# Kernel tuning notes

Measured on AMD Instinct MI355X. Metric: run time of the kernel, lower is better.

The kernel has to match this reference:

```python
import jax, jax.numpy as jnp
import numpy as np

N = 50000
E = 1600000
D_CONTENT, D_STYLE, D_CAT = 768, 128, 32  # concat feature = 2*D_CAT = 64
H1, H2, NCLS = 64, 64, 2


def _lin_params(key, din, dout, bias=True):
    k1, k2 = jax.random.split(key)
    s = 1.0 / np.sqrt(din)
    W = jax.random.uniform(k1, (din, dout), jnp.float32, -s, s)
    b = jax.random.uniform(k2, (dout,), jnp.float32, -s, s) if bias else None
    return W, b


def setup_inputs() -> dict:
    key = jax.random.key(0)
    ks = jax.random.split(key, 16)
    x_content = jax.random.normal(ks[0], (N, D_CONTENT), jnp.float32)
    x_style = jax.random.normal(ks[1], (N, D_STYLE), jnp.float32)
    edge_index = jax.random.randint(ks[2], (2, E), 0, N, jnp.int64)
    edge_type = jax.random.randint(ks[3], (E,), 0, 4, jnp.int64)
    Wp, bp = _lin_params(ks[4], D_CONTENT, D_CAT)
    Ws, bs = _lin_params(ks[5], D_STYLE, D_CAT)
    # SAGEConv: lin_l (aggregated neighbors, has bias), lin_r (root, no bias)
    Wl1, bl1 = _lin_params(ks[6], 2 * D_CAT, H1)
    Wr1, _ = _lin_params(ks[7], 2 * D_CAT, H1, bias=False)
    Wl2, bl2 = _lin_params(ks[8], H1, H2)
    Wr2, _ = _lin_params(ks[9], H1, H2, bias=False)
    Wl3, bl3 = _lin_params(ks[10], H2, H2)
    Wr3, _ = _lin_params(ks[11], H2, H2, bias=False)
    Wo, bo = _lin_params(ks[12], H2, NCLS)
    return dict(x_content=x_content, x_style=x_style, edge_index=edge_index,
                edge_type=edge_type, Wp=Wp, bp=bp, Ws=Ws, bs=bs,
                Wl1=Wl1, bl1=bl1, Wr1=Wr1, Wl2=Wl2, bl2=bl2, Wr2=Wr2,
                Wl3=Wl3, bl3=bl3, Wr3=Wr3, Wo=Wo, bo=bo)


def _sage_conv(x, src, dst, Wl, bl, Wr):
    # mean aggregation of source-node features at destination nodes
    msg_sum = jax.ops.segment_sum(x[src], dst, num_segments=N)  # [N, d]
    deg = jax.ops.segment_sum(jnp.ones((src.shape[0],), x.dtype), dst,
                              num_segments=N)
    agg = msg_sum / jnp.maximum(deg, 1.0)[:, None]
    return agg @ Wl + bl + x @ Wr


def reference(x_content, x_style, edge_index, edge_type,
              Wp, bp, Ws, bs, Wl1, bl1, Wr1, Wl2, bl2, Wr2,
              Wl3, bl3, Wr3, Wo, bo):
    src, dst = edge_index[0], edge_index[1]
    x = jnp.concatenate([x_content @ Wp + bp, x_style @ Ws + bs], axis=1)
    x = jax.nn.relu(_sage_conv(x, src, dst, Wl1, bl1, Wr1))  # dropout = id (eval)
    x = jax.nn.relu(_sage_conv(x, src, dst, Wl2, bl2, Wr2))
    x = jax.nn.relu(_sage_conv(x, src, dst, Wl3, bl3, Wr3))
    return x @ Wo + bo
```

## Files before the change

### kernel.cpp

```cpp
#include <hip/hip_runtime.h>
#include <stdint.h>


typedef __attribute__((ext_vector_type(8))) unsigned short u16x8;
typedef __attribute__((ext_vector_type(4))) float f32x4;

static __device__ __forceinline__ float bf2f(unsigned short u) {
  union { unsigned int i; float f; } v;
  v.i = ((unsigned int)u) << 16;
  return v.f;
}

static __device__ __forceinline__ unsigned short f2bf(float f) {
  union { float f; unsigned int i; } v;
  v.f = f;
  unsigned int u = v.i;
  unsigned int r = (u + 0x7FFFu + ((u >> 16) & 1u)) >> 16;
  return (unsigned short)r;
}

template <bool BF>
static __device__ __forceinline__ float ldf(const void* p, long long i) {
  if (BF) return bf2f(((const unsigned short*)p)[i]);
  return ((const float*)p)[i];
}

template <bool BF>
static __device__ __forceinline__ void loadw8q(const void* p, int row, int q,
                                               float* wv) {
  if (BF) {
    const unsigned int* d = (const unsigned int*)p + row * 16 + q * 4;
#pragma unroll
    for (int t = 0; t < 4; ++t) {
      unsigned int u = d[t];
      union { unsigned int i; float f; } c0, c1;
      c0.i = u << 16;
      c1.i = u & 0xFFFF0000u;
      wv[2 * t + 0] = c0.f;
      wv[2 * t + 1] = c1.f;
    }
  } else {
    const float* d = (const float*)p + row * 32 + q * 8;
#pragma unroll
    for (int t = 0; t < 8; ++t) wv[t] = d[t];
  }
}

static __device__ __forceinline__ int clampN(int v, int N) {
  return v < 0 ? 0 : (v >= N ? N - 1 : v);
}

__global__ void k_detect(const void* Wp, const int* ei, int* flags) {
  if (threadIdx.x == 0 && blockIdx.x == 0) {
    const unsigned short* w = (const unsigned short*)Wp;
    int bf = 1;
    for (int i = 0; i < 64; ++i) {
      float v = fabsf(bf2f(w[i]));
      if (!(v < 1.0f)) bf = 0;
    }
    flags[0] = bf;
    int i64 = 1;
    for (int i = 0; i < 32; ++i)
      if (ei[2 * i + 1] != 0) i64 = 0;
    flags[1] = i64;
  }
}

static __device__ __forceinline__ int edge_src(const int* ei, int e, int E,
                                               int i64) {
  return i64 ? ei[2 * (long long)e] : ei[e];
}
static __device__ __forceinline__ int edge_dst(const int* ei, int e, int E,
                                               int i64) {
  return i64 ? ei[2 * ((long long)E + e)] : ei[(long long)E + e];
}


__global__ __launch_bounds__(256) void k_deg(const int* __restrict__ ei, int E,
                                             int N, int* __restrict__ cnt,
                                             const int* __restrict__ flags) {
  int e = blockIdx.x * 256 + threadIdx.x;
  if (e < E) {
    int d = clampN(edge_dst(ei, e, E, flags[1]), N);
    atomicAdd(&cnt[d], 1);
  }
}

__global__ __launch_bounds__(256) void k_scan1(const int* __restrict__ cnt,
                                               int* __restrict__ rowptr,
                                               int* __restrict__ bsum, int N) {
  __shared__ int sh[256];
  int t = threadIdx.x;
  int base = blockIdx.x * 1024 + t * 4;
  int v0 = 0, v1 = 0, v2 = 0, v3 = 0;
  if (base + 0 < N) v0 = cnt[base + 0];
  if (base + 1 < N) v1 = cnt[base + 1];
  if (base + 2 < N) v2 = cnt[base + 2];
  if (base + 3 < N) v3 = cnt[base + 3];
  int s = v0 + v1 + v2 + v3;
  sh[t] = s;
  __syncthreads();
  int acc = s;
  for (int off = 1; off < 256; off <<= 1) {
    int x = 0;
    if (t >= off) x = sh[t - off];
    __syncthreads();
    acc += x;
    sh[t] = acc;
    __syncthreads();
  }
  int run = acc - s;
  if (base + 0 < N) rowptr[base + 0] = run;
  run += v0;
  if (base + 1 < N) rowptr[base + 1] = run;
  run += v1;
  if (base + 2 < N) rowptr[base + 2] = run;
  run += v2;
  if (base + 3 < N) rowptr[base + 3] = run;
  run += v3;
  if (t == 255) bsum[blockIdx.x] = acc;
}

__global__ void k_scan2(int* __restrict__ bsum, int nb,
                        int* __restrict__ rowptr, int N) {
  if (threadIdx.x == 0 && blockIdx.x == 0) {
    int run = 0;
    for (int i = 0; i < nb; ++i) {
      int v = bsum[i];
      bsum[i] = run;
      run += v;
    }
    rowptr[N] = run;
  }
}

__global__ __launch_bounds__(256) void k_scan3(int* __restrict__ rowptr,
                                               int* __restrict__ cursor,
                                               const int* __restrict__ bsum,
                                               int N) {
  int i = blockIdx.x * 256 + threadIdx.x;
  if (i < N) {
    int v = rowptr[i] + bsum[i >> 10];
    rowptr[i] = v;
    cursor[i] = v;
  }
}

__global__ __launch_bounds__(256) void k_scatter(const int* __restrict__ ei,
                                                 int E, int N,
                                                 int* __restrict__ cursor,
                                                 int* __restrict__ colbuf,
                                                 const int* __restrict__ flags) {
  int e = blockIdx.x * 256 + threadIdx.x;
  if (e < E) {
    int i64 = flags[1];
    int s = clampN(edge_src(ei, e, E, i64), N);
    int d = clampN(edge_dst(ei, e, E, i64), N);
    int p = atomicAdd(&cursor[d], 1);
    if (p >= 0 && p < E) colbuf[p] = s;
  }
}

template <bool BF>
static __device__ void project_body(const void* __restrict__ xc,
                                    const void* __restrict__ xs,
                                    const void* __restrict__ Wp,
                                    const void* __restrict__ bp,
                                    const void* __restrict__ Ws,
                                    const void* __restrict__ bs,
                                    float* __restrict__ h0, int N,
                                    float* __restrict__ xt) {
  int tid = (int)threadIdx.x;
  int w = __builtin_amdgcn_readfirstlane(tid >> 6);
  int lane = tid & 63;
  int node = (int)blockIdx.x * 64 + lane;

  int sn = tid >> 2;
  int sj = tid & 3;
  int gsn = (int)blockIdx.x * 64 + sn;
  int gsnc = gsn < N ? gsn : (N - 1);

  float c[8], s[8];
#pragma unroll
  for (int r = 0; r < 8; ++r) {
    c[r] = 0.f;
    s[r] = 0.f;
  }

  u16x8 pr0 = {}, pr1 = {};
  f32x4 pf0 = {}, pf1 = {}, pf2 = {}, pf3 = {};

  auto stage_load = [&](int t) {
    long long idx;
    const void* src;
    if (t < 12) {
      src = xc;
      idx = (long long)gsnc * 768 + t * 64 + 16 * sj;
    } else {
      src = xs;
      idx = (long long)gsnc * 128 + (t - 12) * 64 + 16 * sj;
    }
    if (BF) {
      const unsigned short* p = (const unsigned short*)src + idx;
      pr0 = *(const u16x8*)p;
      pr1 = *(const u16x8*)(p + 8);
    } else {
      const float* p = (const float*)src + idx;
      pf0 = *(const f32x4*)(p + 0);
      pf1 = *(const f32x4*)(p + 4);
      pf2 = *(const f32x4*)(p + 8);
      pf3 = *(const f32x4*)(p + 12);
    }
  };

  auto stage_write = [&](int t) {
    float* row = xt + (t & 1) * (64 * 65) + sn * 65 + 16 * sj;
    if (BF) {
#pragma unroll
      for (int i = 0; i < 8; ++i) row[i] = bf2f(pr0[i]);
#pragma unroll
      for (int i = 0; i < 8; ++i) row[8 + i] = bf2f(pr1[i]);
    } else {
#pragma unroll
      for (int i = 0; i < 4; ++i) {
        row[i] = pf0[i];
        row[4 + i] = pf1[i];
        row[8 + i] = pf2[i];
        row[12 + i] = pf3[i];
      }
    }
  };

  stage_load(0);
  stage_write(0);
  __syncthreads();

#pragma unroll 1
  for (int t = 0; t < 14; ++t) {
    if (t + 1 < 14) stage_load(t + 1);

    const float* xrow = xt + (t & 1) * (64 * 65) + lane * 65;
    if (t < 12) {
      int rbase = t * 64;
#pragma unroll 1
      for (int k0 = 0; k0 < 64; k0 += 8) {
#pragma unroll
        for (int kk = 0; kk < 8; ++kk) {
          float xv = xrow[k0 + kk];
          float wv[8];
          loadw8q<BF>(Wp, rbase + k0 + kk, w, wv);
#pragma unroll
          for (int r = 0; r < 8; ++r) c[r] += xv * wv[r];
        }
      }
    } else {
      int rbase = (t - 12) * 64;
#pragma unroll 1
      for (int k0 = 0; k0 < 64; k0 += 8) {
#pragma unroll
        for (int kk = 0; kk < 8; ++kk) {
          float xv = xrow[k0 + kk];
          float wv[8];
          loadw8q<BF>(Ws, rbase + k0 + kk, w, wv);
#pragma unroll
          for (int r = 0; r < 8; ++r) s[r] += xv * wv[r];
        }
      }
    }

    if (t + 1 < 14) stage_write(t + 1);
    __syncthreads();
  }

  if (node < N) {
    float* orow = h0 + (long long)node * 64;
    f32x4 v;
#pragma unroll
    for (int r = 0; r < 4; ++r) v[r] = c[r] + ldf<BF>(bp, 8 * w + r);
    *(f32x4*)(orow + 8 * w) = v;
#pragma unroll
    for (int r = 0; r < 4; ++r) v[r] = c[4 + r] + ldf<BF>(bp, 8 * w + 4 + r);
    *(f32x4*)(orow + 8 * w + 4) = v;
#pragma unroll
    for (int r = 0; r < 4; ++r) v[r] = s[r] + ldf<BF>(bs, 8 * w + r);
    *(f32x4*)(orow + 32 + 8 * w) = v;
#pragma unroll
    for (int r = 0; r < 4; ++r) v[r] = s[4 + r] + ldf<BF>(bs, 8 * w + 4 + r);
    *(f32x4*)(orow + 32 + 8 * w + 4) = v;
  }
}

__global__ __launch_bounds__(256) void k_project(
    const void* __restrict__ xc, const void* __restrict__ xs,
    const void* __restrict__ Wp, const void* __restrict__ bp,
    const void* __restrict__ Ws, const void* __restrict__ bs,
    float* __restrict__ h0, int N, const int* __restrict__ flags) {
  __shared__ float xt[2 * 64 * 65];
  if (flags[0])
    project_body<true>(xc, xs, Wp, bp, Ws, bs, h0, N, xt);
  else
    project_body<false>(xc, xs, Wp, bp, Ws, bs, h0, N, xt);
}

template <bool BF>
static __device__ void layer_body(const float* __restrict__ hin,
                                  const int* __restrict__ rowptr,
                                  const int* __restrict__ colbuf,
                                  const void* Wl, const void* bl,
                                  const void* Wr, float* __restrict__ hout,
                                  int N, int last, const void* Wo,
                                  const void* bo, void* outp) {
  int node = (int)((blockIdx.x * blockDim.x + threadIdx.x) >> 6);
  int lane = (int)(threadIdx.x & 63);
  if (node >= N) return;
  int rs = rowptr[node], re = rowptr[node + 1];
  float xself = hin[(long long)node * 64 + lane];
  float agg0 = 0.f, agg1 = 0.f, agg2 = 0.f, agg3 = 0.f;
  float agg4 = 0.f, agg5 = 0.f, agg6 = 0.f, agg7 = 0.f;
  for (int cb = rs; cb < re; cb += 64) {
    int sidx = 0;
    if (cb + lane < re) sidx = clampN(colbuf[cb + lane], N);
    int c = re - cb;
    if (c > 64) c = 64;
    int t = 0;
    for (; t + 8 <= c; t += 8) {
      int s0 = __builtin_amdgcn_readlane(sidx, t + 0);
      int s1 = __builtin_amdgcn_readlane(sidx, t + 1);
      int s2 = __builtin_amdgcn_readlane(sidx, t + 2);
      int s3 = __builtin_amdgcn_readlane(sidx, t + 3);
      int s4 = __builtin_amdgcn_readlane(sidx, t + 4);
      int s5 = __builtin_amdgcn_readlane(sidx, t + 5);
      int s6 = __builtin_amdgcn_readlane(sidx, t + 6);
      int s7 = __builtin_amdgcn_readlane(sidx, t + 7);
      float v0 = hin[(long long)s0 * 64 + lane];
      float v1 = hin[(long long)s1 * 64 + lane];
      float v2 = hin[(long long)s2 * 64 + lane];
      float v3 = hin[(long long)s3 * 64 + lane];
      float v4 = hin[(long long)s4 * 64 + lane];
      float v5 = hin[(long long)s5 * 64 + lane];
      float v6 = hin[(long long)s6 * 64 + lane];
      float v7 = hin[(long long)s7 * 64 + lane];
      agg0 += v0;
      agg1 += v1;
      agg2 += v2;
      agg3 += v3;
      agg4 += v4;
      agg5 += v5;
      agg6 += v6;
      agg7 += v7;
    }
    for (; t < c; ++t) {
      int s = __builtin_amdgcn_readlane(sidx, t);
      agg0 += hin[(long long)s * 64 + lane];
    }
  }
  float agg = ((agg0 + agg1) + (agg2 + agg3)) + ((agg4 + agg5) + (agg6 + agg7));
  int deg = re - rs;
  if (deg > 0) agg *= (1.f / (float)deg);

  float o = ldf<BF>(bl, lane);
#pragma unroll 8
  for (int d = 0; d < 64; ++d) {
    float ad = __uint_as_float(
        __builtin_amdgcn_readlane(__float_as_uint(agg), d));
    float xd = __uint_as_float(
        __builtin_amdgcn_readlane(__float_as_uint(xself), d));
    o += ad * ldf<BF>(Wl, d * 64 + lane);
    o += xd * ldf<BF>(Wr, d * 64 + lane);
  }
  o = fmaxf(o, 0.f);

  if (!last) {
    hout[(long long)node * 64 + lane] = o;
  } else {
    float c0 = o * ldf<BF>(Wo, lane * 2 + 0);
    float c1 = o * ldf<BF>(Wo, lane * 2 + 1);
    for (int off = 32; off > 0; off >>= 1) {
      c0 += __shfl_xor(c0, off, 64);
      c1 += __shfl_xor(c1, off, 64);
    }
    if (lane == 0) {
      float r0 = c0 + ldf<BF>(bo, 0);
      float r1 = c1 + ldf<BF>(bo, 1);
      if (BF) {
        unsigned short* o16 = (unsigned short*)outp;
        o16[(long long)node * 2 + 0] = f2bf(r0);
        o16[(long long)node * 2 + 1] = f2bf(r1);
      } else {
        float* o32 = (float*)outp;
        o32[(long long)node * 2 + 0] = r0;
        o32[(long long)node * 2 + 1] = r1;
      }
    }
  }
}

__global__ __launch_bounds__(256) void k_layer(
    const float* hin, const int* rowptr, const int* colbuf, const void* Wl,
    const void* bl, const void* Wr, float* hout, int N, int last,
    const void* Wo, const void* bo, void* outp, const int* __restrict__ flags) {
  if (flags[0])
    layer_body<true>(hin, rowptr, colbuf, Wl, bl, Wr, hout, N, last, Wo, bo,
                     outp);
  else
    layer_body<false>(hin, rowptr, colbuf, Wl, bl, Wr, hout, N, last, Wo, bo,
                      outp);
}


extern "C" void kernel_launch(void* const* d_in, const int* in_sizes, int n_in,
                              void* d_out, int out_size, void* d_ws,
                              size_t ws_size, hipStream_t stream) {
  const void* xc = d_in[0];
  const void* xs = d_in[1];
  const int* ei = (const int*)d_in[2];
  const void* Wp = d_in[4];
  const void* bp = d_in[5];
  const void* Ws = d_in[6];
  const void* bs = d_in[7];
  const void* Wl1 = d_in[8];
  const void* bl1 = d_in[9];
  const void* Wr1 = d_in[10];
  const void* Wl2 = d_in[11];
  const void* bl2 = d_in[12];
  const void* Wr2 = d_in[13];
  const void* Wl3 = d_in[14];
  const void* bl3 = d_in[15];
  const void* Wr3 = d_in[16];
  const void* Wo = d_in[17];
  const void* bo = d_in[18];

  int N = out_size / 2;
  int E = in_sizes[3];

  char* ws = (char*)d_ws;
  size_t off = 0;
  auto alloc = [&](size_t bytes) {
    char* p = ws + off;
    off += (bytes + 255) & ~(size_t)255;
    return p;
  };
  int* colbuf = (int*)alloc((size_t)E * 4);
  int* cnt = (int*)alloc((size_t)N * 4);
  int* rowptr = (int*)alloc((size_t)(N + 1) * 4);
  int* cursor = (int*)alloc((size_t)N * 4);
  int* bsum = (int*)alloc(4096);
  int* flags = (int*)alloc(256);
  float* h0 = (float*)alloc((size_t)N * 64 * 4);
  float* h1 = (float*)alloc((size_t)N * 64 * 4);
  (void)ws_size;
  (void)n_in;

  k_detect<<<1, 64, 0, stream>>>(Wp, ei, flags);

  hipMemsetAsync(cnt, 0, (size_t)N * 4, stream);
  int eb = (E + 255) / 256;
  k_deg<<<eb, 256, 0, stream>>>(ei, E, N, cnt, flags);
  int sb = (N + 1023) / 1024;
  k_scan1<<<sb, 256, 0, stream>>>(cnt, rowptr, bsum, N);
  k_scan2<<<1, 64, 0, stream>>>(bsum, sb, rowptr, N);
  k_scan3<<<(N + 255) / 256, 256, 0, stream>>>(rowptr, cursor, bsum, N);
  k_scatter<<<eb, 256, 0, stream>>>(ei, E, N, cursor, colbuf, flags);

  int pb = (N + 63) / 64;
  k_project<<<pb, 256, 0, stream>>>(xc, xs, Wp, bp, Ws, bs, h0, N, flags);

  int nb4 = (N + 3) / 4;
  k_layer<<<nb4, 256, 0, stream>>>(h0, rowptr, colbuf, Wl1, bl1, Wr1, h1, N, 0,
                                   nullptr, nullptr, nullptr, flags);
  k_layer<<<nb4, 256, 0, stream>>>(h1, rowptr, colbuf, Wl2, bl2, Wr2, h0, N, 0,
                                   nullptr, nullptr, nullptr, flags);
  k_layer<<<nb4, 256, 0, stream>>>(h0, rowptr, colbuf, Wl3, bl3, Wr3, h1, N, 1,
                                   Wo, bo, d_out, flags);
}
```

Baseline: 786.9 us.

## Stage projection weight tiles in LDS and vectorize LDS reads in project kernel

The projection kernel now loads each 64-row weight tile cooperatively into double-buffered LDS alongside the input tile, instead of having every wavefront read weights directly from global memory per k step. The input tile row stride changes from 65 to 68 floats so rows can be written and read as 16-byte vectors, and the inner loop reads four x values and a packed weight vector per step. This targets the global/scalar load latency on the weight path and the cost of scalar LDS accesses, at the price of more LDS per block, which may reduce occupancy, and possible bank conflicts from the padding of 68.

```diff
diff --git a/kernel.cpp b/kernel.cpp
--- a/kernel.cpp
+++ b/kernel.cpp
@@ -4,6 +4,7 @@
 
 typedef __attribute__((ext_vector_type(8))) unsigned short u16x8;
 typedef __attribute__((ext_vector_type(4))) float f32x4;
+typedef __attribute__((ext_vector_type(4))) unsigned int u32x4;
 
 static __device__ __forceinline__ float bf2f(unsigned short u) {
   union { unsigned int i; float f; } v;
@@ -23,27 +24,6 @@
 static __device__ __forceinline__ float ldf(const void* p, long long i) {
   if (BF) return bf2f(((const unsigned short*)p)[i]);
   return ((const float*)p)[i];
-}
-
-template <bool BF>
-static __device__ __forceinline__ void loadw8q(const void* p, int row, int q,
-                                               float* wv) {
-  if (BF) {
-    const unsigned int* d = (const unsigned int*)p + row * 16 + q * 4;
-#pragma unroll
-    for (int t = 0; t < 4; ++t) {
-      unsigned int u = d[t];
-      union { unsigned int i; float f; } c0, c1;
-      c0.i = u << 16;
-      c1.i = u & 0xFFFF0000u;
-      wv[2 * t + 0] = c0.f;
-      wv[2 * t + 1] = c1.f;
-    }
-  } else {
-    const float* d = (const float*)p + row * 32 + q * 8;
-#pragma unroll
-    for (int t = 0; t < 8; ++t) wv[t] = d[t];
-  }
 }
 
 static __device__ __forceinline__ int clampN(int v, int N) {
@@ -169,7 +149,11 @@
                                     const void* __restrict__ Ws,
                                     const void* __restrict__ bs,
                                     float* __restrict__ h0, int N,
-                                    float* __restrict__ xt) {
+                                    float* __restrict__ lds) {
+  float* xt = lds;
+  unsigned int* wtb = (unsigned int*)(lds + 2 * 64 * 68);
+  float* wtf = lds + 2 * 64 * 68;
+
   int tid = (int)threadIdx.x;
   int w = __builtin_amdgcn_readfirstlane(tid >> 6);
   int lane = tid & 63;
@@ -189,6 +173,8 @@
 
   u16x8 pr0 = {}, pr1 = {};
   f32x4 pf0 = {}, pf1 = {}, pf2 = {}, pf3 = {};
+  u32x4 wrg = {};
+  f32x4 wf0 = {}, wf1 = {};
 
   auto stage_load = [&](int t) {
     long long idx;
@@ -211,23 +197,46 @@
       pf2 = *(const f32x4*)(p + 8);
       pf3 = *(const f32x4*)(p + 12);
     }
+    int rowg = (t < 12) ? (t * 64 + sn) : ((t - 12) * 64 + sn);
+    const void* wsrc = (t < 12) ? Wp : Ws;
+    if (BF) {
+      wrg = *(const u32x4*)((const unsigned int*)wsrc +
+                            (long long)rowg * 16 + 4 * sj);
+    } else {
+      const float* p = (const float*)wsrc + (long long)rowg * 32 + 8 * sj;
+      wf0 = *(const f32x4*)p;
+      wf1 = *(const f32x4*)(p + 4);
+    }
   };
 
   auto stage_write = [&](int t) {
-    float* row = xt + (t & 1) * (64 * 65) + sn * 65 + 16 * sj;
+    float* row = xt + (t & 1) * (64 * 68) + sn * 68 + 16 * sj;
     if (BF) {
-#pragma unroll
-      for (int i = 0; i < 8; ++i) row[i] = bf2f(pr0[i]);
-#pragma unroll
-      for (int i = 0; i < 8; ++i) row[8 + i] = bf2f(pr1[i]);
+      f32x4 v;
+#pragma unroll
+      for (int i = 0; i < 4; ++i) v[i] = bf2f(pr0[i]);
+      *(f32x4*)(row + 0) = v;
+#pragma unroll
+      for (int i = 0; i < 4; ++i) v[i] = bf2f(pr0[4 + i]);
+      *(f32x4*)(row + 4) = v;
+#pragma unroll
+      for (int i = 0; i < 4; ++i) v[i] = bf2f(pr1[i]);
+      *(f32x4*)(row + 8) = v;
+#pragma unroll
+      for (int i = 0; i < 4; ++i) v[i] = bf2f(pr1[4 + i]);
+      *(f32x4*)(row + 12) = v;
     } else {
-#pragma unroll
-      for (int i = 0; i < 4; ++i) {
-        row[i] = pf0[i];
-        row[4 + i] = pf1[i];
-        row[8 + i] = pf2[i];
-        row[12 + i] = pf3[i];
-      }
+      *(f32x4*)(row + 0) = pf0;
+      *(f32x4*)(row + 4) = pf1;
+      *(f32x4*)(row + 8) = pf2;
+      *(f32x4*)(row + 12) = pf3;
+    }
+    if (BF) {
+      *(u32x4*)(wtb + (t & 1) * (64 * 16) + sn * 16 + 4 * sj) = wrg;
+    } else {
+      float* wrow = wtf + (t & 1) * (64 * 32) + sn * 32 + 8 * sj;
+      *(f32x4*)wrow = wf0;
+      *(f32x4*)(wrow + 4) = wf1;
     }
   };
 
@@ -239,31 +248,77 @@
   for (int t = 0; t < 14; ++t) {
     if (t + 1 < 14) stage_load(t + 1);
 
-    const float* xrow = xt + (t & 1) * (64 * 65) + lane * 65;
-    if (t < 12) {
-      int rbase = t * 64;
-#pragma unroll 1
-      for (int k0 = 0; k0 < 64; k0 += 8) {
-#pragma unroll
-        for (int kk = 0; kk < 8; ++kk) {
-          float xv = xrow[k0 + kk];
-          float wv[8];
-          loadw8q<BF>(Wp, rbase + k0 + kk, w, wv);
-#pragma unroll
-          for (int r = 0; r < 8; ++r) c[r] += xv * wv[r];
+    const float* xrow = xt + (t & 1) * (64 * 68) + lane * 68;
+    if (BF) {
+      const unsigned int* wbase = wtb + (t & 1) * (64 * 16) + 4 * w;
+      if (t < 12) {
+#pragma unroll 2
+        for (int k0 = 0; k0 < 64; k0 += 4) {
+          f32x4 x4 = *(const f32x4*)(xrow + k0);
+#pragma unroll
+          for (int kk = 0; kk < 4; ++kk) {
+            u32x4 wp4 = *(const u32x4*)(wbase + (k0 + kk) * 16);
+#pragma unroll
+            for (int p = 0; p < 4; ++p) {
+              union { unsigned int i; float f; } lo, hi;
+              lo.i = wp4[p] << 16;
+              hi.i = wp4[p] & 0xFFFF0000u;
+              c[2 * p + 0] += x4[kk] * lo.f;
+              c[2 * p + 1] += x4[kk] * hi.f;
+            }
+          }
+        }
+      } else {
+#pragma unroll 2
+        for (int k0 = 0; k0 < 64; k0 += 4) {
+          f32x4 x4 = *(const f32x4*)(xrow + k0);
+#pragma unroll
+          for (int kk = 0; kk < 4; ++kk) {
+            u32x4 wp4 = *(const u32x4*)(wbase + (k0 + kk) * 16);
+#pragma unroll
+            for (int p = 0; p < 4; ++p) {
+              union { unsigned int i; float f; } lo, hi;
+              lo.i = wp4[p] << 16;
+              hi.i = wp4[p] & 0xFFFF0000u;
+              s[2 * p + 0] += x4[kk] * lo.f;
+              s[2 * p + 1] += x4[kk] * hi.f;
+            }
+          }
         }
       }
     } else {
-      int rbase = (t - 12) * 64;
-#pragma unroll 1
-      for (int k0 = 0; k0 < 64; k0 += 8) {
-#pragma unroll
-        for (int kk = 0; kk < 8; ++kk) {
-          float xv = xrow[k0 + kk];
-          float wv[8];
-          loadw8q<BF>(Ws, rbase + k0 + kk, w, wv);
-#pragma unroll
-          for (int r = 0; r < 8; ++r) s[r] += xv * wv[r];
+      const float* wbase = wtf + (t & 1) * (64 * 32) + 8 * w;
+      if (t < 12) {
+#pragma unroll 2
+        for (int k0 = 0; k0 < 64; k0 += 4) {
+          f32x4 x4 = *(const f32x4*)(xrow + k0);
+#pragma unroll
+          for (int kk = 0; kk < 4; ++kk) {
+            const float* wr = wbase + (k0 + kk) * 32;
+            f32x4 wa = *(const f32x4*)wr;
+            f32x4 wb = *(const f32x4*)(wr + 4);
+#pragma unroll
+            for (int r = 0; r < 4; ++r) {
+              c[r] += x4[kk] * wa[r];
+              c[4 + r] += x4[kk] * wb[r];
+            }
+          }
+        }
+      } else {
+#pragma unroll 2
+        for (int k0 = 0; k0 < 64; k0 += 4) {
+          f32x4 x4 = *(const f32x4*)(xrow + k0);
+#pragma unroll
+          for (int kk = 0; kk < 4; ++kk) {
+            const float* wr = wbase + (k0 + kk) * 32;
+            f32x4 wa = *(const f32x4*)wr;
+            f32x4 wb = *(const f32x4*)(wr + 4);
+#pragma unroll
+            for (int r = 0; r < 4; ++r) {
+              s[r] += x4[kk] * wa[r];
+              s[4 + r] += x4[kk] * wb[r];
+            }
+          }
         }
       }
     }
@@ -295,11 +350,11 @@
     const void* __restrict__ Wp, const void* __restrict__ bp,
     const void* __restrict__ Ws, const void* __restrict__ bs,
     float* __restrict__ h0, int N, const int* __restrict__ flags) {
-  __shared__ float xt[2 * 64 * 65];
+  __shared__ float lds[2 * 64 * 68 + 2 * 64 * 32];
   if (flags[0])
-    project_body<true>(xc, xs, Wp, bp, Ws, bs, h0, N, xt);
+    project_body<true>(xc, xs, Wp, bp, Ws, bs, h0, N, lds);
   else
-    project_body<false>(xc, xs, Wp, bp, Ws, bs, h0, N, xt);
+    project_body<false>(xc, xs, Wp, bp, Ws, bs, h0, N, lds);
 }
 
 template <bool BF>
```

Measured after the change: 743.4 us. 5.5% less time.
